# Optimization experiments

Measured on AMD Instinct MI355X. Metric: run time of the kernel, lower is better.

## Reference

```python
import jax, jax.numpy as jnp
import numpy as np

NUM_HEADS = 16
HEAD_DIM = 128
ROT_DIM = 128  # rotary_emb_dim == head_dim
ROPE_BASE = 10000.0


def setup_inputs() -> dict:
    key = jax.random.key(0)
    k1, k2, k3, k4, k5 = jax.random.split(key, 5)
    b, s, d = 2, 2048, 2048
    return {
        "x": jax.random.normal(k1, (b, s, d), jnp.float32),
        "Wqkv_w": jax.random.normal(k2, (3 * d, d), jnp.float32) * (d ** -0.5),
        "Wqkv_b": jax.random.normal(k3, (3 * d,), jnp.float32) * 0.02,
        "wo_w": jax.random.normal(k4, (d, d), jnp.float32) * (d ** -0.5),
        "wo_b": jax.random.normal(k5, (d,), jnp.float32) * 0.02,
    }


def _deinterleave(t):
    # torch.cat([t[..., ::2], t[..., 1::2]], dim=-1)
    return jnp.concatenate([t[..., ::2], t[..., 1::2]], axis=-1)


def _rope(t, cos, sin):
    # non-interleaved (GPT-NeoX style) rotary on first ROT_DIM dims; here ROT_DIM == head_dim
    half = ROT_DIM // 2
    x1, x2 = t[..., :half], t[..., half:ROT_DIM]
    # cos/sin: (s, half) -> broadcast over (b, s, h, half)
    c = cos[None, :, None, :]
    sn = sin[None, :, None, :]
    return jnp.concatenate([x1 * c - x2 * sn, x2 * c + x1 * sn], axis=-1)


def reference(x, Wqkv_w, Wqkv_b, wo_w, wo_b):
    b, s, d = x.shape
    h, hd = NUM_HEADS, HEAD_DIM
    # fused QKV projection, layout '(h three d)' per original rearrange
    qkv = x @ Wqkv_w.T + Wqkv_b                      # (b, s, 3*d)
    qkv = qkv.reshape(b, s, h, 3, hd)
    q = _deinterleave(qkv[:, :, :, 0, :])            # (b, s, h, hd)
    k = _deinterleave(qkv[:, :, :, 1, :])
    v = qkv[:, :, :, 2, :]
    # rotary embedding tables
    inv_freq = 1.0 / (ROPE_BASE ** (jnp.arange(0, ROT_DIM, 2, dtype=jnp.float32) / ROT_DIM))
    freqs = jnp.arange(s, dtype=jnp.float32)[:, None] * inv_freq[None, :]  # (s, half)
    cos, sin = jnp.cos(freqs), jnp.sin(freqs)
    q = _rope(q, cos, sin)
    k = _rope(k, cos, sin)
    # causal self-attention (SelfAttention, softmax_scale = 1/sqrt(hd))
    scale = hd ** -0.5
    scores = jnp.einsum('bshd,bthd->bhst', q, k) * scale  # (b, h, s, s)
    mask = jnp.tril(jnp.ones((s, s), dtype=bool))
    scores = jnp.where(mask[None, None], scores, jnp.finfo(scores.dtype).min)
    probs = jax.nn.softmax(scores, axis=-1)
    ctx = jnp.einsum('bhst,bthd->bshd', probs, v)    # (b, s, h, hd)
    ctx = ctx.reshape(b, s, d)
    return ctx @ wo_w.T + wo_b
```

## Files before the change

kernel.cpp:

```cpp
#include <hip/hip_runtime.h>

#define B_ 2
#define S_ 2048
#define H_ 16
#define HD_ 128
#define QKVROW 6144
#define M_ 4096

typedef float f32x4 __attribute__((ext_vector_type(4)));
typedef __bf16 bf16x8 __attribute__((ext_vector_type(8)));
typedef unsigned short ushortx8 __attribute__((ext_vector_type(8)));

__device__ __forceinline__ float bf2f(unsigned short u) {
  union { unsigned u; float f; } v;
  v.u = ((unsigned)u) << 16;
  return v.f;
}
__device__ __forceinline__ unsigned short f2bf(float f) {
  union { __bf16 b; unsigned short u; } c;
  c.b = (__bf16)f;
  return c.u;
}
__device__ __forceinline__ ushortx8 cvt8(const float* f) {
  const f32x4 lo = *(const f32x4*)f;
  const f32x4 hi = *(const f32x4*)(f + 4);
  ushortx8 o;
#pragma unroll
  for (int t = 0; t < 4; ++t) o[t] = f2bf(lo[t]);
#pragma unroll
  for (int t = 0; t < 4; ++t) o[4 + t] = f2bf(hi[t]);
  return o;
}
__device__ __forceinline__ void async16(const unsigned short* g, unsigned short* l) {
  __builtin_amdgcn_global_load_lds(
      (const __attribute__((address_space(1))) unsigned int*)g,
      (__attribute__((address_space(3))) unsigned int*)l, 16, 0, 0);
}

__global__ __launch_bounds__(256) void f2bf_arr(
    const float* __restrict__ src, unsigned short* __restrict__ dst, int n8) {
  int i = blockIdx.x * 256 + threadIdx.x;
  const int stride = gridDim.x * 256;
  for (; i < n8; i += stride) {
    const ushortx8 o = cvt8(src + (size_t)i * 8);
    *(ushortx8*)&dst[(size_t)i * 8] = o;
  }
}

__global__ __launch_bounds__(256) void gemm1(
    const unsigned short* __restrict__ A, const unsigned short* __restrict__ Bm,
    const float* __restrict__ bias, unsigned short* __restrict__ C) {
  __shared__ unsigned short As[128 * 64];
  __shared__ unsigned short Bs[128 * 64];
  const int tid = threadIdx.x;
  const int lane = tid & 63, wave = tid >> 6;
  const int l15 = lane & 15, quad = lane >> 4;
  const int m0 = blockIdx.y * 128, n0 = blockIdx.x * 128;
  const int wr = (wave >> 1) * 64, wc = (wave & 1) * 64;

  f32x4 acc[4][4];
#pragma unroll
  for (int r = 0; r < 4; ++r)
#pragma unroll
    for (int c = 0; c < 4; ++c) acc[r][c] = (f32x4){0.f, 0.f, 0.f, 0.f};

  for (int k0 = 0; k0 < 2048; k0 += 64) {
    __syncthreads();
#pragma unroll
    for (int i = 0; i < 4; ++i) {
      const int c0 = wave * 256 + i * 64;
      const int u = c0 + lane;
      const int row = u >> 3, cu = u & 7;
      const int cs = cu ^ (row & 7);
      async16(A + (size_t)(m0 + row) * 2048 + k0 + cs * 8, &As[c0 * 8]);
      async16(Bm + (size_t)(n0 + row) * 2048 + k0 + cs * 8, &Bs[c0 * 8]);
    }
    __syncthreads();

#pragma unroll
    for (int s = 0; s < 2; ++s) {
      bf16x8 af[4], bf[4];
#pragma unroll
      for (int r = 0; r < 4; ++r) {
        const int row = wr + r * 16 + l15;
        af[r] = *(const bf16x8*)&As[row * 64 + (((s * 4 + quad) ^ (row & 7)) << 3)];
      }
#pragma unroll
      for (int c = 0; c < 4; ++c) {
        const int row = wc + c * 16 + l15;
        bf[c] = *(const bf16x8*)&Bs[row * 64 + (((s * 4 + quad) ^ (row & 7)) << 3)];
      }
#pragma unroll
      for (int r = 0; r < 4; ++r)
#pragma unroll
        for (int c = 0; c < 4; ++c)
          acc[r][c] = __builtin_amdgcn_mfma_f32_16x16x32_bf16(af[r], bf[c], acc[r][c], 0, 0, 0);
    }
  }

#pragma unroll
  for (int c = 0; c < 4; ++c) {
    const int col = n0 + wc + c * 16 + l15;
    const float bv = bias[col];
#pragma unroll
    for (int r = 0; r < 4; ++r) {
      const int row = m0 + wr + r * 16 + quad * 4;
#pragma unroll
      for (int i = 0; i < 4; ++i)
        C[(size_t)(row + i) * QKVROW + col] = f2bf(acc[r][c][i] + bv);
    }
  }
}

__global__ __launch_bounds__(256) void rope_vt(
    unsigned short* qkv, unsigned short* __restrict__ Vt) {
  __shared__ unsigned short vs[64 * 136];
  const int b = blockIdx.z, h = blockIdx.y, s0 = blockIdx.x * 64;
  const int tid = threadIdx.x;
  const int r = tid >> 2, cpart = (tid & 3) * 32;
  const int s = s0 + r;
  unsigned short* base = qkv + (size_t)(b * S_ + s) * QKVROW + h * 384;
  const int j0 = cpart >> 1;

  ushortx8 ivq[4], ivk[4], ivv[4];
#pragma unroll
  for (int i = 0; i < 4; ++i) {
    ivq[i] = *(const ushortx8*)&base[cpart + i * 8];
    ivk[i] = *(const ushortx8*)&base[128 + cpart + i * 8];
    ivv[i] = *(const ushortx8*)&base[256 + cpart + i * 8];
  }

  float cs[16], sn[16];
#pragma unroll
  for (int t = 0; t < 16; ++t) {
    const float invf = expf(-(float)(j0 + t) * 0.14391156831212787f);
    sincosf((float)s * invf, &sn[t], &cs[t]);
  }

  __syncthreads();

#pragma unroll
  for (int which = 0; which < 2; ++which) {
    const ushortx8* iv = (which == 0) ? ivq : ivk;
    const float scale = (which == 0) ? 0.08838834764831845f : 1.0f;
    ushortx8 o1a, o1b, o2a, o2b;
#pragma unroll
    for (int t = 0; t < 16; ++t) {
      const float x1 = bf2f(iv[(2 * t) >> 3][(2 * t) & 7]);
      const float x2 = bf2f(iv[(2 * t + 1) >> 3][(2 * t + 1) & 7]);
      const unsigned short r1 = f2bf((x1 * cs[t] - x2 * sn[t]) * scale);
      const unsigned short r2 = f2bf((x2 * cs[t] + x1 * sn[t]) * scale);
      if (t < 8) { o1a[t] = r1; o2a[t] = r2; }
      else       { o1b[t - 8] = r1; o2b[t - 8] = r2; }
    }
    unsigned short* out = base + which * 128;
    *(ushortx8*)&out[j0] = o1a;
    *(ushortx8*)&out[j0 + 8] = o1b;
    *(ushortx8*)&out[64 + j0] = o2a;
    *(ushortx8*)&out[64 + j0 + 8] = o2b;
  }

#pragma unroll
  for (int i = 0; i < 4; ++i)
    *(ushortx8*)&vs[r * 136 + cpart + i * 8] = ivv[i];
  __syncthreads();
  const size_t vtb = (size_t)(b * H_ + h) * HD_ * S_ + s0;
#pragma unroll
  for (int it = 0; it < 4; ++it) {
    const int a = tid + it * 256;
    const int d = a >> 3, sc = (a & 7) * 8;
    ushortx8 o;
#pragma unroll
    for (int t = 0; t < 8; ++t) o[t] = vs[(sc + t) * 136 + d];
    *(ushortx8*)&Vt[vtb + (size_t)d * S_ + sc] = o;
  }
}

__global__ __launch_bounds__(512) void attn(
    unsigned short* qkv, const unsigned short* __restrict__ Vt) {
  __shared__ unsigned short Ks[64 * 136];
  __shared__ unsigned short Vs[128 * 72];
  __shared__ unsigned short Ps[8 * 16 * 72];
  const int p = blockIdx.x, bh = blockIdx.y;
  const int b = bh >> 4, h = bh & 15;
  const int tid = threadIdx.x, lane = tid & 63, wave = tid >> 6;
  const int l15 = lane & 15, quad = lane >> 4;

  unsigned short* qh = qkv + (size_t)b * S_ * QKVROW + h * 384;
  const unsigned short* Vb = Vt + (size_t)bh * HD_ * S_;
  unsigned short* Pw = &Ps[wave * 16 * 72];

  ushortx8 rk[2], rv[2];
  auto pref = [&](int j) {
#pragma unroll
    for (int t = 0; t < 2; ++t) {
      const int uk = t * 512 + tid;
      const int krow = uk >> 4, kcu = uk & 15;
      rk[t] = *(const ushortx8*)(qh + (size_t)(j * 64 + krow) * QKVROW + 128 + kcu * 8);
      const int vrow = uk >> 3, vcu = uk & 7;
      rv[t] = *(const ushortx8*)(Vb + (size_t)vrow * S_ + j * 64 + vcu * 8);
    }
  };
  pref(0);

#pragma unroll
  for (int half = 0; half < 2; ++half) {
    const int qt = half ? 15 - p : p;
    const int jN = 2 * qt + 2;

    bf16x8 aq[4];
#pragma unroll
    for (int ks = 0; ks < 4; ++ks)
      aq[ks] = *(const bf16x8*)&qh[(size_t)(qt * 128 + wave * 16 + l15) * QKVROW +
                                   ks * 32 + quad * 8];

    f32x4 o[8];
    float mrow[4], lrow[4];
#pragma unroll
    for (int ct = 0; ct < 8; ++ct) o[ct] = (f32x4){0.f, 0.f, 0.f, 0.f};
#pragma unroll
    for (int i = 0; i < 4; ++i) { mrow[i] = -1e30f; lrow[i] = 0.f; }

    for (int j = 0; j < jN; ++j) {
      __syncthreads();
#pragma unroll
      for (int t = 0; t < 2; ++t) {
        const int uk = t * 512 + tid;
        *(ushortx8*)&Ks[(uk >> 4) * 136 + (uk & 15) * 8] = rk[t];
        *(ushortx8*)&Vs[(uk >> 3) * 72 + (uk & 7) * 8] = rv[t];
      }
      __syncthreads();

      const int jn = (j + 1 < jN) ? j + 1 : (half == 0 ? 0 : -1);
      if (jn >= 0) pref(jn);

      f32x4 sacc[4];
#pragma unroll
      for (int ct = 0; ct < 4; ++ct) sacc[ct] = (f32x4){0.f, 0.f, 0.f, 0.f};
#pragma unroll
      for (int ks = 0; ks < 4; ++ks) {
        bf16x8 bk[4];
#pragma unroll
        for (int ct = 0; ct < 4; ++ct)
          bk[ct] = *(const bf16x8*)&Ks[(ct * 16 + l15) * 136 + ks * 32 + quad * 8];
#pragma unroll
        for (int ct = 0; ct < 4; ++ct)
          sacc[ct] = __builtin_amdgcn_mfma_f32_16x16x32_bf16(aq[ks], bk[ct], sacc[ct], 0, 0, 0);
      }

      if (j >= 2 * qt) {
#pragma unroll
        for (int ct = 0; ct < 4; ++ct)
#pragma unroll
          for (int i = 0; i < 4; ++i) {
            const int grow = qt * 128 + wave * 16 + quad * 4 + i;
            const int gcol = j * 64 + ct * 16 + l15;
            if (gcol > grow) sacc[ct][i] = -1e30f;
          }
      }

#pragma unroll
      for (int i = 0; i < 4; ++i) {
        float m = sacc[0][i];
#pragma unroll
        for (int ct = 1; ct < 4; ++ct) m = fmaxf(m, sacc[ct][i]);
#pragma unroll
        for (int off = 1; off < 16; off <<= 1) m = fmaxf(m, __shfl_xor(m, off));
        const float mn = fmaxf(mrow[i], m);
        const float alpha = __expf(mrow[i] - mn);
        mrow[i] = mn;
        float rsum = 0.f;
#pragma unroll
        for (int ct = 0; ct < 4; ++ct) {
          const float pv = __expf(sacc[ct][i] - mn);
          sacc[ct][i] = pv;
          rsum += pv;
        }
#pragma unroll
        for (int off = 1; off < 16; off <<= 1) rsum += __shfl_xor(rsum, off);
        lrow[i] = lrow[i] * alpha + rsum;
#pragma unroll
        for (int ct = 0; ct < 8; ++ct) o[ct][i] *= alpha;
      }

#pragma unroll
      for (int ct = 0; ct < 4; ++ct)
#pragma unroll
        for (int i = 0; i < 4; ++i)
          Pw[(quad * 4 + i) * 72 + ct * 16 + l15] = f2bf(sacc[ct][i]);

#pragma unroll
      for (int ks = 0; ks < 2; ++ks) {
        const bf16x8 ap = *(const bf16x8*)&Pw[l15 * 72 + ks * 32 + quad * 8];
        bf16x8 bv[8];
#pragma unroll
        for (int ct = 0; ct < 8; ++ct)
          bv[ct] = *(const bf16x8*)&Vs[(ct * 16 + l15) * 72 + ks * 32 + quad * 8];
#pragma unroll
        for (int ct = 0; ct < 8; ++ct)
          o[ct] = __builtin_amdgcn_mfma_f32_16x16x32_bf16(ap, bv[ct], o[ct], 0, 0, 0);
      }
    }

    float inv[4];
#pragma unroll
    for (int i = 0; i < 4; ++i) inv[i] = 1.0f / lrow[i];
#pragma unroll
    for (int ct = 0; ct < 8; ++ct)
#pragma unroll
      for (int i = 0; i < 4; ++i) {
        const int srow = qt * 128 + wave * 16 + quad * 4 + i;
        qh[(size_t)srow * QKVROW + ct * 16 + l15] = f2bf(o[ct][i] * inv[i]);
      }
  }
}

__global__ __launch_bounds__(256) void gemm2(
    const unsigned short* __restrict__ A, const unsigned short* __restrict__ Bm,
    const float* __restrict__ bias, float* __restrict__ C) {
  __shared__ unsigned short As[128 * 64];
  __shared__ unsigned short Bs[128 * 64];
  const int tid = threadIdx.x;
  const int lane = tid & 63, wave = tid >> 6;
  const int l15 = lane & 15, quad = lane >> 4;
  const int m0 = blockIdx.y * 128, n0 = blockIdx.x * 128;
  const int wr = (wave >> 1) * 64, wc = (wave & 1) * 64;

  f32x4 acc[4][4];
#pragma unroll
  for (int r = 0; r < 4; ++r)
#pragma unroll
    for (int c = 0; c < 4; ++c) acc[r][c] = (f32x4){0.f, 0.f, 0.f, 0.f};

  for (int k0 = 0; k0 < 2048; k0 += 64) {
    const int kh = ((k0 >> 7) * 384) + (k0 & 127);
    __syncthreads();
#pragma unroll
    for (int i = 0; i < 4; ++i) {
      const int c0 = wave * 256 + i * 64;
      const int u = c0 + lane;
      const int row = u >> 3, cu = u & 7;
      const int cs = cu ^ (row & 7);
      async16(A + (size_t)(m0 + row) * QKVROW + kh + cs * 8, &As[c0 * 8]);
      async16(Bm + (size_t)(n0 + row) * 2048 + k0 + cs * 8, &Bs[c0 * 8]);
    }
    __syncthreads();

#pragma unroll
    for (int s = 0; s < 2; ++s) {
      bf16x8 af[4], bf[4];
#pragma unroll
      for (int r = 0; r < 4; ++r) {
        const int row = wr + r * 16 + l15;
        af[r] = *(const bf16x8*)&As[row * 64 + (((s * 4 + quad) ^ (row & 7)) << 3)];
      }
#pragma unroll
      for (int c = 0; c < 4; ++c) {
        const int row = wc + c * 16 + l15;
        bf[c] = *(const bf16x8*)&Bs[row * 64 + (((s * 4 + quad) ^ (row & 7)) << 3)];
      }
#pragma unroll
      for (int r = 0; r < 4; ++r)
#pragma unroll
        for (int c = 0; c < 4; ++c)
          acc[r][c] = __builtin_amdgcn_mfma_f32_16x16x32_bf16(af[r], bf[c], acc[r][c], 0, 0, 0);
    }
  }

#pragma unroll
  for (int c = 0; c < 4; ++c) {
    const int col = n0 + wc + c * 16 + l15;
    const float bv = bias[col];
#pragma unroll
    for (int r = 0; r < 4; ++r) {
      const int row = m0 + wr + r * 16 + quad * 4;
#pragma unroll
      for (int i = 0; i < 4; ++i)
        C[(size_t)(row + i) * 2048 + col] = acc[r][c][i] + bv;
    }
  }
}

extern "C" void kernel_launch(void* const* d_in, const int* in_sizes, int n_in,
                              void* d_out, int out_size, void* d_ws, size_t ws_size,
                              hipStream_t stream) {
  const float* x    = (const float*)d_in[0];
  const float* wqkv = (const float*)d_in[1];
  const float* bqkv = (const float*)d_in[2];
  const float* wo   = (const float*)d_in[3];
  const float* bo   = (const float*)d_in[4];
  float* out = (float*)d_out;

  unsigned short* qkv = (unsigned short*)d_ws;
  unsigned short* Vt  = qkv + (size_t)M_ * QKVROW;
  unsigned short* xb  = Vt  + (size_t)B_ * H_ * HD_ * S_;
  unsigned short* wb  = xb  + (size_t)M_ * 2048;
  unsigned short* wob = wb  + (size_t)QKVROW * 2048;

  f2bf_arr<<<dim3(2048), 256, 0, stream>>>(x,    xb,  (M_ * 2048) / 8);
  f2bf_arr<<<dim3(2048), 256, 0, stream>>>(wqkv, wb,  (QKVROW * 2048) / 8);
  f2bf_arr<<<dim3(1024), 256, 0, stream>>>(wo,   wob, (2048 * 2048) / 8);

  gemm1<<<dim3(QKVROW / 128, M_ / 128), 256, 0, stream>>>(xb, wb, bqkv, qkv);
  rope_vt<<<dim3(S_ / 64, H_, B_), 256, 0, stream>>>(qkv, Vt);
  attn<<<dim3(8, B_ * H_), 512, 0, stream>>>(qkv, Vt);
  gemm2<<<dim3(2048 / 128, M_ / 128), 256, 0, stream>>>(qkv, wob, bo, out);
}
```

Before: 413.9 us.

## Double-buffer GEMM tiles with async prefetch, larger 256x128 tiles, fuse conversion kernels

Both projection GEMMs now use 512-thread blocks with 256x128 output tiles and a two-stage LDS double buffer. The next k-tile is prefetched with async global-to-LDS loads while the current one is consumed, with explicit vmcnt waits and scheduling barriers plus setprio around the MFMA bursts. The three fp32-to-bf16 conversion launches are merged into one kernel. The aim is to hide global load latency and cut launch overhead, at the cost of 96KB LDS per block and lower occupancy; fewer blocks for gemm2 (256) may underfill the GPU.

```diff
diff --git a/kernel.cpp b/kernel.cpp
--- a/kernel.cpp
+++ b/kernel.cpp
@@ -37,78 +37,124 @@
       (__attribute__((address_space(3))) unsigned int*)l, 16, 0, 0);
 }
 
-__global__ __launch_bounds__(256) void f2bf_arr(
-    const float* __restrict__ src, unsigned short* __restrict__ dst, int n8) {
+#define SBAR()                                  \
+  do {                                          \
+    __builtin_amdgcn_sched_barrier(0);          \
+    __builtin_amdgcn_s_barrier();               \
+    __builtin_amdgcn_sched_barrier(0);          \
+  } while (0)
+
+__global__ __launch_bounds__(256) void f2bf3(
+    const float* __restrict__ a, unsigned short* __restrict__ da, int na8,
+    const float* __restrict__ b, unsigned short* __restrict__ db, int nb8,
+    const float* __restrict__ c, unsigned short* __restrict__ dc, int nc8) {
+  const int ntot = na8 + nb8 + nc8;
   int i = blockIdx.x * 256 + threadIdx.x;
   const int stride = gridDim.x * 256;
-  for (; i < n8; i += stride) {
-    const ushortx8 o = cvt8(src + (size_t)i * 8);
-    *(ushortx8*)&dst[(size_t)i * 8] = o;
-  }
-}
-
-__global__ __launch_bounds__(256) void gemm1(
+  for (; i < ntot; i += stride) {
+    const float* s;
+    unsigned short* d;
+    int off = i;
+    if (off < na8) { s = a; d = da; }
+    else if (off - na8 < nb8) { off -= na8; s = b; d = db; }
+    else { off -= na8 + nb8; s = c; d = dc; }
+    const ushortx8 o = cvt8(s + (size_t)off * 8);
+    *(ushortx8*)&d[(size_t)off * 8] = o;
+  }
+}
+
+__global__ __launch_bounds__(512) void gemm1(
     const unsigned short* __restrict__ A, const unsigned short* __restrict__ Bm,
     const float* __restrict__ bias, unsigned short* __restrict__ C) {
-  __shared__ unsigned short As[128 * 64];
-  __shared__ unsigned short Bs[128 * 64];
+  __shared__ unsigned short As[2][256 * 64];
+  __shared__ unsigned short Bs[2][128 * 64];
   const int tid = threadIdx.x;
   const int lane = tid & 63, wave = tid >> 6;
   const int l15 = lane & 15, quad = lane >> 4;
-  const int m0 = blockIdx.y * 128, n0 = blockIdx.x * 128;
-  const int wr = (wave >> 1) * 64, wc = (wave & 1) * 64;
-
-  f32x4 acc[4][4];
-#pragma unroll
-  for (int r = 0; r < 4; ++r)
-#pragma unroll
-    for (int c = 0; c < 4; ++c) acc[r][c] = (f32x4){0.f, 0.f, 0.f, 0.f};
-
-  for (int k0 = 0; k0 < 2048; k0 += 64) {
-    __syncthreads();
-#pragma unroll
-    for (int i = 0; i < 4; ++i) {
-      const int c0 = wave * 256 + i * 64;
-      const int u = c0 + lane;
+  const int wm = wave >> 2, wn = wave & 3;
+  const int m0 = blockIdx.y * 256, n0 = blockIdx.x * 128;
+
+  f32x4 acc[2][4][2];
+#pragma unroll
+  for (int ph = 0; ph < 2; ++ph)
+#pragma unroll
+    for (int r = 0; r < 4; ++r)
+#pragma unroll
+      for (int c = 0; c < 2; ++c) acc[ph][r][c] = (f32x4){0.f, 0.f, 0.f, 0.f};
+
+  auto stage = [&](int t, int b) {
+#pragma unroll
+    for (int a = 0; a < 4; ++a) {
+      const int u = a * 512 + tid;
       const int row = u >> 3, cu = u & 7;
       const int cs = cu ^ (row & 7);
-      async16(A + (size_t)(m0 + row) * 2048 + k0 + cs * 8, &As[c0 * 8]);
-      async16(Bm + (size_t)(n0 + row) * 2048 + k0 + cs * 8, &Bs[c0 * 8]);
-    }
-    __syncthreads();
-
-#pragma unroll
-    for (int s = 0; s < 2; ++s) {
-      bf16x8 af[4], bf[4];
+      async16(A + (size_t)(m0 + row) * 2048 + t * 64 + cs * 8,
+              &As[b][(a * 512 + wave * 64) * 8]);
+    }
+#pragma unroll
+    for (int a = 0; a < 2; ++a) {
+      const int u = a * 512 + tid;
+      const int row = u >> 3, cu = u & 7;
+      const int cs = cu ^ (row & 7);
+      async16(Bm + (size_t)(n0 + row) * 2048 + t * 64 + cs * 8,
+              &Bs[b][(a * 512 + wave * 64) * 8]);
+    }
+  };
+
+  stage(0, 0);
+  stage(1, 1);
+
+  for (int kt = 0; kt < 32; ++kt) {
+    const int b = kt & 1;
+    if (kt < 30) asm volatile("s_waitcnt vmcnt(6)" ::: "memory");
+    else         asm volatile("s_waitcnt vmcnt(0)" ::: "memory");
+    SBAR();
+
+#pragma unroll
+    for (int ph = 0; ph < 2; ++ph) {
+      bf16x8 af[4][2], bf[2][2];
+#pragma unroll
+      for (int s = 0; s < 2; ++s) {
+#pragma unroll
+        for (int r = 0; r < 4; ++r) {
+          const int row = wm * 128 + ph * 64 + r * 16 + l15;
+          af[r][s] = *(const bf16x8*)&As[b][row * 64 + (((s * 4 + quad) ^ (row & 7)) << 3)];
+        }
+#pragma unroll
+        for (int c = 0; c < 2; ++c) {
+          const int row = wn * 32 + c * 16 + l15;
+          bf[c][s] = *(const bf16x8*)&Bs[b][row * 64 + (((s * 4 + quad) ^ (row & 7)) << 3)];
+        }
+      }
+      __builtin_amdgcn_s_setprio(1);
+#pragma unroll
+      for (int s = 0; s < 2; ++s)
+#pragma unroll
+        for (int r = 0; r < 4; ++r)
+#pragma unroll
+          for (int c = 0; c < 2; ++c)
+            acc[ph][r][c] = __builtin_amdgcn_mfma_f32_16x16x32_bf16(
+                af[r][s], bf[c][s], acc[ph][r][c], 0, 0, 0);
+      __builtin_amdgcn_s_setprio(0);
+      SBAR();
+    }
+
+    if (kt + 2 < 32) stage(kt + 2, b);
+  }
+
+#pragma unroll
+  for (int c = 0; c < 2; ++c) {
+    const int col = n0 + wn * 32 + c * 16 + l15;
+    const float bv = bias[col];
+#pragma unroll
+    for (int ph = 0; ph < 2; ++ph)
 #pragma unroll
       for (int r = 0; r < 4; ++r) {
-        const int row = wr + r * 16 + l15;
-        af[r] = *(const bf16x8*)&As[row * 64 + (((s * 4 + quad) ^ (row & 7)) << 3)];
-      }
-#pragma unroll
-      for (int c = 0; c < 4; ++c) {
-        const int row = wc + c * 16 + l15;
-        bf[c] = *(const bf16x8*)&Bs[row * 64 + (((s * 4 + quad) ^ (row & 7)) << 3)];
-      }
-#pragma unroll
-      for (int r = 0; r < 4; ++r)
-#pragma unroll
-        for (int c = 0; c < 4; ++c)
-          acc[r][c] = __builtin_amdgcn_mfma_f32_16x16x32_bf16(af[r], bf[c], acc[r][c], 0, 0, 0);
-    }
-  }
-
-#pragma unroll
-  for (int c = 0; c < 4; ++c) {
-    const int col = n0 + wc + c * 16 + l15;
-    const float bv = bias[col];
-#pragma unroll
-    for (int r = 0; r < 4; ++r) {
-      const int row = m0 + wr + r * 16 + quad * 4;
-#pragma unroll
-      for (int i = 0; i < 4; ++i)
-        C[(size_t)(row + i) * QKVROW + col] = f2bf(acc[r][c][i] + bv);
-    }
+        const int row = m0 + wm * 128 + ph * 64 + r * 16 + quad * 4;
+#pragma unroll
+        for (int i = 0; i < 4; ++i)
+          C[(size_t)(row + i) * QKVROW + col] = f2bf(acc[ph][r][c][i] + bv);
+      }
   }
 }
 
@@ -315,69 +361,99 @@
   }
 }
 
-__global__ __launch_bounds__(256) void gemm2(
+__global__ __launch_bounds__(512) void gemm2(
     const unsigned short* __restrict__ A, const unsigned short* __restrict__ Bm,
     const float* __restrict__ bias, float* __restrict__ C) {
-  __shared__ unsigned short As[128 * 64];
-  __shared__ unsigned short Bs[128 * 64];
+  __shared__ unsigned short As[2][256 * 64];
+  __shared__ unsigned short Bs[2][128 * 64];
   const int tid = threadIdx.x;
   const int lane = tid & 63, wave = tid >> 6;
   const int l15 = lane & 15, quad = lane >> 4;
-  const int m0 = blockIdx.y * 128, n0 = blockIdx.x * 128;
-  const int wr = (wave >> 1) * 64, wc = (wave & 1) * 64;
-
-  f32x4 acc[4][4];
-#pragma unroll
-  for (int r = 0; r < 4; ++r)
-#pragma unroll
-    for (int c = 0; c < 4; ++c) acc[r][c] = (f32x4){0.f, 0.f, 0.f, 0.f};
-
-  for (int k0 = 0; k0 < 2048; k0 += 64) {
-    const int kh = ((k0 >> 7) * 384) + (k0 & 127);
-    __syncthreads();
-#pragma unroll
-    for (int i = 0; i < 4; ++i) {
-      const int c0 = wave * 256 + i * 64;
-      const int u = c0 + lane;
+  const int wm = wave >> 2, wn = wave & 3;
+  const int m0 = blockIdx.y * 256, n0 = blockIdx.x * 128;
+
+  f32x4 acc[2][4][2];
+#pragma unroll
+  for (int ph = 0; ph < 2; ++ph)
+#pragma unroll
+    for (int r = 0; r < 4; ++r)
+#pragma unroll
+      for (int c = 0; c < 2; ++c) acc[ph][r][c] = (f32x4){0.f, 0.f, 0.f, 0.f};
+
+  auto stage = [&](int t, int b) {
+    const int kh = ((t >> 1) * 384) + ((t & 1) * 64);
+#pragma unroll
+    for (int a = 0; a < 4; ++a) {
+      const int u = a * 512 + tid;
       const int row = u >> 3, cu = u & 7;
       const int cs = cu ^ (row & 7);
-      async16(A + (size_t)(m0 + row) * QKVROW + kh + cs * 8, &As[c0 * 8]);
-      async16(Bm + (size_t)(n0 + row) * 2048 + k0 + cs * 8, &Bs[c0 * 8]);
-    }
-    __syncthreads();
-
-#pragma unroll
-    for (int s = 0; s < 2; ++s) {
-      bf16x8 af[4], bf[4];
+      async16(A + (size_t)(m0 + row) * QKVROW + kh + cs * 8,
+              &As[b][(a * 512 + wave * 64) * 8]);
+    }
+#pragma unroll
+    for (int a = 0; a < 2; ++a) {
+      const int u = a * 512 + tid;
+      const int row = u >> 3, cu = u & 7;
+      const int cs = cu ^ (row & 7);
+      async16(Bm + (size_t)(n0 + row) * 2048 + t * 64 + cs * 8,
+              &Bs[b][(a * 512 + wave * 64) * 8]);
+    }
+  };
+
+  stage(0, 0);
+  stage(1, 1);
+
+  for (int kt = 0; kt < 32; ++kt) {
+    const int b = kt & 1;
+    if (kt < 30) asm volatile("s_waitcnt vmcnt(6)" ::: "memory");
+    else         asm volatile("s_waitcnt vmcnt(0)" ::: "memory");
+    SBAR();
+
+#pragma unroll
+    for (int ph = 0; ph < 2; ++ph) {
+      bf16x8 af[4][2], bf[2][2];
+#pragma unroll
+      for (int s = 0; s < 2; ++s) {
+#pragma unroll
+        for (int r = 0; r < 4; ++r) {
+          const int row = wm * 128 + ph * 64 + r * 16 + l15;
+          af[r][s] = *(const bf16x8*)&As[b][row * 64 + (((s * 4 + quad) ^ (row & 7)) << 3)];
+        }
+#pragma unroll
+        for (int c = 0; c < 2; ++c) {
+          const int row = wn * 32 + c * 16 + l15;
+          bf[c][s] = *(const bf16x8*)&Bs[b][row * 64 + (((s * 4 + quad) ^ (row & 7)) << 3)];
+        }
+      }
+      __builtin_amdgcn_s_setprio(1);
+#pragma unroll
+      for (int s = 0; s < 2; ++s)
+#pragma unroll
+        for (int r = 0; r < 4; ++r)
+#pragma unroll
+          for (int c = 0; c < 2; ++c)
+            acc[ph][r][c] = __builtin_amdgcn_mfma_f32_16x16x32_bf16(
+                af[r][s], bf[c][s], acc[ph][r][c], 0, 0, 0);
+      __builtin_amdgcn_s_setprio(0);
+      SBAR();
+    }
+
+    if (kt + 2 < 32) stage(kt + 2, b);
+  }
+
+#pragma unroll
+  for (int c = 0; c < 2; ++c) {
+    const int col = n0 + wn * 32 + c * 16 + l15;
+    const float bv = bias[col];
+#pragma unroll
+    for (int ph = 0; ph < 2; ++ph)
 #pragma unroll
       for (int r = 0; r < 4; ++r) {
-        const int row = wr + r * 16 + l15;
-        af[r] = *(const bf16x8*)&As[row * 64 + (((s * 4 + quad) ^ (row & 7)) << 3)];
-      }
-#pragma unroll
-      for (int c = 0; c < 4; ++c) {
-        const int row = wc + c * 16 + l15;
-        bf[c] = *(const bf16x8*)&Bs[row * 64 + (((s * 4 + quad) ^ (row & 7)) << 3)];
-      }
-#pragma unroll
-      for (int r = 0; r < 4; ++r)
-#pragma unroll
-        for (int c = 0; c < 4; ++c)
-          acc[r][c] = __builtin_amdgcn_mfma_f32_16x16x32_bf16(af[r], bf[c], acc[r][c], 0, 0, 0);
-    }
-  }
-
-#pragma unroll
-  for (int c = 0; c < 4; ++c) {
-    const int col = n0 + wc + c * 16 + l15;
-    const float bv = bias[col];
-#pragma unroll
-    for (int r = 0; r < 4; ++r) {
-      const int row = m0 + wr + r * 16 + quad * 4;
-#pragma unroll
-      for (int i = 0; i < 4; ++i)
-        C[(size_t)(row + i) * 2048 + col] = acc[r][c][i] + bv;
-    }
+        const int row = m0 + wm * 128 + ph * 64 + r * 16 + quad * 4;
+#pragma unroll
+        for (int i = 0; i < 4; ++i)
+          C[(size_t)(row + i) * 2048 + col] = acc[ph][r][c][i] + bv;
+      }
   }
 }
 
@@ -397,12 +473,12 @@
   unsigned short* wb  = xb  + (size_t)M_ * 2048;
   unsigned short* wob = wb  + (size_t)QKVROW * 2048;
 
-  f2bf_arr<<<dim3(2048), 256, 0, stream>>>(x,    xb,  (M_ * 2048) / 8);
-  f2bf_arr<<<dim3(2048), 256, 0, stream>>>(wqkv, wb,  (QKVROW * 2048) / 8);
-  f2bf_arr<<<dim3(1024), 256, 0, stream>>>(wo,   wob, (2048 * 2048) / 8);
-
-  gemm1<<<dim3(QKVROW / 128, M_ / 128), 256, 0, stream>>>(xb, wb, bqkv, qkv);
+  f2bf3<<<dim3(2048), 256, 0, stream>>>(x, xb, (M_ * 2048) / 8,
+                                        wqkv, wb, (QKVROW * 2048) / 8,
+                                        wo, wob, (2048 * 2048) / 8);
+
+  gemm1<<<dim3(QKVROW / 128, M_ / 256), 512, 0, stream>>>(xb, wb, bqkv, qkv);
   rope_vt<<<dim3(S_ / 64, H_, B_), 256, 0, stream>>>(qkv, Vt);
   attn<<<dim3(8, B_ * H_), 512, 0, stream>>>(qkv, Vt);
-  gemm2<<<dim3(2048 / 128, M_ / 128), 256, 0, stream>>>(qkv, wob, bo, out);
-}
+  gemm2<<<dim3(2048 / 128, M_ / 256), 512, 0, stream>>>(qkv, wob, bo, out);
+}
```

After: 444.6 us. 7.4% more time.
